# Optimization experiments

Measured on AMD Instinct MI355X. Metric: run time of the kernel, lower is better.

The kernel has to match this reference:

```python
import jax, jax.numpy as jnp
import numpy as np

D_K = 64

def setup_inputs() -> dict:
    key = jax.random.key(0)
    kq, kk, kv = jax.random.split(key, 3)
    shape = (2, 16, 2048, D_K)  # [B, H, S, d_k]
    q = jax.random.normal(kq, shape, dtype=jnp.float32)
    k = jax.random.normal(kk, shape, dtype=jnp.float32)
    v = jax.random.normal(kv, shape, dtype=jnp.float32)
    return {"q": q, "k": k, "v": v}

def reference(q, k, v):
    # score = q @ k^T / sqrt(d_k)  -> [B, H, S, S]
    scale = 1.0 / np.sqrt(D_K).astype(np.float32)
    score = jnp.einsum("bhqd,bhkd->bhqk", q, k) * scale
    attn = jax.nn.softmax(score, axis=-1)
    # dropout is identity in eval mode
    out = jnp.einsum("bhqk,bhkd->bhqd", attn, v)
    return out
```

## Files before the change

kernel.cpp:

```cpp
#include <hip/hip_runtime.h>
#include <hip/hip_bf16.h>
#include <math.h>
#include <stdint.h>


#define S_LEN 2048
#define DK 64
#define QW 32
#define NW 4
#define QBLK (QW * NW)
#define KVBLK 64
#define NT (S_LEN / KVBLK)
#define LOG2E 1.44269504088896340736f
#define THR 8.0f

typedef __attribute__((ext_vector_type(16))) float f32x16;
typedef __attribute__((ext_vector_type(8)))  __bf16 bf16x8;
typedef __attribute__((ext_vector_type(4)))  __bf16 bf16x4;
typedef __attribute__((ext_vector_type(4)))  uint32_t u32x4;

union frag_cast { u32x4 u; bf16x8 h; };

__device__ __forceinline__ uint32_t cvt_pk_bf16(float lo, float hi) {
    uint32_t r;
    asm("v_cvt_pk_bf16_f32 %0, %1, %2" : "=v"(r) : "v"(lo), "v"(hi));
    return r;
}
__device__ __forceinline__ void perm32swap(uint32_t& a, uint32_t& b) {
    asm volatile("v_permlane32_swap_b32 %0, %1" : "+v"(a), "+v"(b));
}
__device__ __forceinline__ void load_lds16(const __bf16* g, __bf16* l) {
    __builtin_amdgcn_global_load_lds(
        (const __attribute__((address_space(1))) void*)g,
        (__attribute__((address_space(3))) void*)l, 16, 0, 0);
}
__device__ __forceinline__ bf16x8 pack8(float4 a, float4 b) {
    bf16x8 f;
    f[0] = (__bf16)a.x; f[1] = (__bf16)a.y; f[2] = (__bf16)a.z; f[3] = (__bf16)a.w;
    f[4] = (__bf16)b.x; f[5] = (__bf16)b.y; f[6] = (__bf16)b.z; f[7] = (__bf16)b.w;
    return f;
}

__global__ __launch_bounds__(256)
void prep_pack(const float* __restrict__ Kg, const float* __restrict__ Vg,
               __bf16* __restrict__ Kimg, __bf16* __restrict__ Vimg)
{
    __shared__ float Vs[64 * 65];
    const int tid = threadIdx.x;
    const int t = blockIdx.x, bh = blockIdx.y;
    const size_t ibase = ((size_t)bh * S_LEN + (size_t)t * 64) * DK;
    const size_t obase = ((size_t)bh * NT + t) * 4096;

    #pragma unroll
    for (int u = 0; u < 2; ++u) {
        const int rho = tid + 256 * u;
        const int r = rho >> 3, j = rho & 7;
        const float* src = Kg + ibase + r * 64 + j * 8;
        float4 a = *(const float4*)(src);
        float4 b = *(const float4*)(src + 4);
        *(bf16x8*)(Kimg + obase + r * 64 + ((j * 8) ^ ((r & 7) << 3))) = pack8(a, b);
    }

    {
        const int r = tid >> 2, c0 = (tid & 3) * 16;
        const float* src = Vg + ibase + r * 64 + c0;
        #pragma unroll
        for (int m = 0; m < 4; ++m) {
            float4 x = *(const float4*)(src + 4 * m);
            float* dst = &Vs[r * 65 + c0 + 4 * m];
            dst[0] = x.x; dst[1] = x.y; dst[2] = x.z; dst[3] = x.w;
        }
    }
    __syncthreads();
    #pragma unroll
    for (int u = 0; u < 2; ++u) {
        const int rho = tid + 256 * u;
        const int d = rho >> 3, j = rho & 7;
        const int k0 = 8 * (j ^ (d & 7));
        bf16x8 wv;
        #pragma unroll
        for (int i = 0; i < 8; ++i) wv[i] = (__bf16)Vs[(k0 + i) * 65 + d];
        *(bf16x8*)(Vimg + obase + d * 64 + j * 8) = wv;
    }
}

__global__ __launch_bounds__(256, 2)
void attn_fwd_lds(const float* __restrict__ Qg, const __bf16* __restrict__ Kimg,
                  const __bf16* __restrict__ Vimg, float* __restrict__ Og)
{
    __shared__ __align__(16) __bf16 Kl[2][4096];
    __shared__ __align__(16) __bf16 Vt[2][4096];

    const int tid = threadIdx.x;
    const int lane = tid & 63;
    const int w   = tid >> 6;
    const int l31 = lane & 31;
    const int hi  = lane >> 5;

    const int qt = blockIdx.x;
    const int bh = blockIdx.y;
    const size_t base = (size_t)bh * (S_LEN * DK);
    const int q0g = qt * QBLK + w * QW;

    bf16x8 qf[4];
    {
        const float sc = 0.125f * LOG2E;
        const float* qrow = Qg + base + (size_t)(q0g + l31) * DK;
        #pragma unroll
        for (int sp = 0; sp < 4; ++sp) {
            const int d0 = 16 * sp + 8 * hi;
            float4 a = *(const float4*)(qrow + d0);
            float4 b = *(const float4*)(qrow + d0 + 4);
            bf16x8 f;
            f[0] = (__bf16)(a.x * sc); f[1] = (__bf16)(a.y * sc);
            f[2] = (__bf16)(a.z * sc); f[3] = (__bf16)(a.w * sc);
            f[4] = (__bf16)(b.x * sc); f[5] = (__bf16)(b.y * sc);
            f[6] = (__bf16)(b.z * sc); f[7] = (__bf16)(b.w * sc);
            qf[sp] = f;
        }
    }

    f32x16 acc0 = {}, acc1 = {};
    float m_run = -INFINITY, l_run = 0.f;

    const __bf16* kbase = Kimg + (size_t)bh * NT * 4096;
    const __bf16* vbase = Vimg + (size_t)bh * NT * 4096;

    auto stage = [&](int t, int b) {
        const __bf16* kt = kbase + (size_t)t * 4096 + tid * 8;
        const __bf16* vt = vbase + (size_t)t * 4096 + tid * 8;
        load_lds16(kt,        &Kl[b][w * 512]);
        load_lds16(kt + 2048, &Kl[b][2048 + w * 512]);
        load_lds16(vt,        &Vt[b][w * 512]);
        load_lds16(vt + 2048, &Vt[b][2048 + w * 512]);
    };

    stage(0, 0);
    __syncthreads();

    int cur = 0;
    #pragma unroll 1
    for (int t = 0; t < NT; ++t) {
        if (t + 1 < NT) stage(t + 1, cur ^ 1);

        f32x16 s0 = {}, s1 = {};
        __builtin_amdgcn_s_setprio(1);
        #pragma unroll
        for (int sp = 0; sp < 4; ++sp) {
            #pragma unroll
            for (int kt2 = 0; kt2 < 2; ++kt2) {
                const int krow = kt2 * 32 + l31;
                const int eo = krow * 64 + ((16 * sp + 8 * hi) ^ ((krow & 7) << 3));
                bf16x8 kb = *(const bf16x8*)(&Kl[cur][eo]);
                if (kt2 == 0) s0 = __builtin_amdgcn_mfma_f32_32x32x16_bf16(kb, qf[sp], s0, 0, 0, 0);
                else          s1 = __builtin_amdgcn_mfma_f32_32x32x16_bf16(kb, qf[sp], s1, 0, 0, 0);
            }
        }
        __builtin_amdgcn_s_setprio(0);

        float vmax = -INFINITY;
        #pragma unroll
        for (int j = 0; j < 16; ++j) vmax = fmaxf(vmax, s0[j]);
        #pragma unroll
        for (int j = 0; j < 16; ++j) vmax = fmaxf(vmax, s1[j]);
        vmax = fmaxf(vmax, __shfl_xor(vmax, 32));

        if (!__all(vmax - m_run <= THR)) {
            const float mnew = fmaxf(m_run, vmax);
            const float alpha = __builtin_amdgcn_exp2f(m_run - mnew);
            m_run = mnew;
            l_run *= alpha;
            #pragma unroll
            for (int r = 0; r < 16; ++r) {
                const int ql = (r & 3) + 8 * (r >> 2) + 4 * hi;
                const float ar = __shfl(alpha, ql + (hi << 5));
                acc0[r] *= ar;
                acc1[r] *= ar;
            }
        }

        float rs = 0.f;
        #pragma unroll
        for (int j = 0; j < 16; ++j) { const float p = __builtin_amdgcn_exp2f(s0[j] - m_run); s0[j] = p; rs += p; }
        #pragma unroll
        for (int j = 0; j < 16; ++j) { const float p = __builtin_amdgcn_exp2f(s1[j] - m_run); s1[j] = p; rs += p; }
        rs += __shfl_xor(rs, 32);
        l_run += rs;

        frag_cast pa[4];
        #pragma unroll
        for (int b2 = 0; b2 < 2; ++b2) {
            #pragma unroll
            for (int st = 0; st < 2; ++st) {
                uint32_t wa, wb, wc, wd;
                if (b2 == 0) {
                    wa = cvt_pk_bf16(s0[8 * st + 0], s0[8 * st + 1]);
                    wb = cvt_pk_bf16(s0[8 * st + 2], s0[8 * st + 3]);
                    wc = cvt_pk_bf16(s0[8 * st + 4], s0[8 * st + 5]);
                    wd = cvt_pk_bf16(s0[8 * st + 6], s0[8 * st + 7]);
                } else {
                    wa = cvt_pk_bf16(s1[8 * st + 0], s1[8 * st + 1]);
                    wb = cvt_pk_bf16(s1[8 * st + 2], s1[8 * st + 3]);
                    wc = cvt_pk_bf16(s1[8 * st + 4], s1[8 * st + 5]);
                    wd = cvt_pk_bf16(s1[8 * st + 6], s1[8 * st + 7]);
                }
                perm32swap(wa, wc);
                perm32swap(wb, wd);
                pa[2 * b2 + st].u = (u32x4){wa, wb, wc, wd};
            }
        }

        __builtin_amdgcn_s_setprio(1);
        #pragma unroll
        for (int ks = 0; ks < 4; ++ks) {
            #pragma unroll
            for (int dt = 0; dt < 2; ++dt) {
                const int d = dt * 32 + l31;
                const int eo = d * 64 + ((16 * ks + 8 * hi) ^ ((d & 7) << 3));
                bf16x8 vb = *(const bf16x8*)(&Vt[cur][eo]);
                if (dt == 0) acc0 = __builtin_amdgcn_mfma_f32_32x32x16_bf16(pa[ks].h, vb, acc0, 0, 0, 0);
                else         acc1 = __builtin_amdgcn_mfma_f32_32x32x16_bf16(pa[ks].h, vb, acc1, 0, 0, 0);
            }
        }
        __builtin_amdgcn_s_setprio(0);

        __syncthreads();
        cur ^= 1;
    }

    float* op = Og + base;
    #pragma unroll
    for (int r = 0; r < 16; ++r) {
        const int ql = (r & 3) + 8 * (r >> 2) + 4 * hi;
        const float lr = __shfl(l_run, ql + (hi << 5));
        const float invl = 1.0f / lr;
        const size_t row = (size_t)(q0g + ql) * DK;
        op[row + l31]      = acc0[r] * invl;
        op[row + 32 + l31] = acc1[r] * invl;
    }
}

__global__ __launch_bounds__(256, 2)
void attn_fwd_fb(const float* __restrict__ Qg, const float* __restrict__ Kg,
                 const float* __restrict__ Vg, float* __restrict__ Og)
{
    __shared__ __align__(16) __bf16 Kl[2][64 * 64];
    __shared__ __align__(16) __bf16 Vt[2][64 * 64];

    const int tid = threadIdx.x;
    const int lane = tid & 63;
    const int w   = tid >> 6;
    const int l31 = lane & 31;
    const int hi  = lane >> 5;

    const int qt = blockIdx.x;
    const int bh = blockIdx.y;
    const size_t base = (size_t)bh * (S_LEN * DK);
    const int q0g = qt * QBLK + w * QW;

    bf16x8 qf[4];
    {
        const float sc = 0.125f * LOG2E;
        const float* qrow = Qg + base + (size_t)(q0g + l31) * DK;
        #pragma unroll
        for (int sp = 0; sp < 4; ++sp) {
            const int d0 = 16 * sp + 8 * hi;
            float4 a = *(const float4*)(qrow + d0);
            float4 b = *(const float4*)(qrow + d0 + 4);
            bf16x8 f;
            f[0] = (__bf16)(a.x * sc); f[1] = (__bf16)(a.y * sc);
            f[2] = (__bf16)(a.z * sc); f[3] = (__bf16)(a.w * sc);
            f[4] = (__bf16)(b.x * sc); f[5] = (__bf16)(b.y * sc);
            f[6] = (__bf16)(b.z * sc); f[7] = (__bf16)(b.w * sc);
            qf[sp] = f;
        }
    }

    f32x16 acc0 = {}, acc1 = {};
    float m_run = -INFINITY, l_run = 0.f;

    float4 kpre[4];
    float  vpre[4][4];
    const int vd  = tid & 63;
    const int vkq = tid >> 6;

    auto issueLoads = [&](int t) {
        const int kv0 = t * KVBLK;
        #pragma unroll
        for (int i = 0; i < 4; ++i) {
            const int idx = tid + 256 * i;
            const int r = idx >> 4, c = idx & 15;
            kpre[i] = *(const float4*)(Kg + base + (size_t)(kv0 + r) * DK + c * 4);
        }
        #pragma unroll
        for (int i = 0; i < 4; ++i) {
            const int k0 = vkq * 4 + 16 * i;
            const float* vp = Vg + base + (size_t)(kv0 + k0) * DK + vd;
            vpre[i][0] = vp[0];      vpre[i][1] = vp[DK];
            vpre[i][2] = vp[2 * DK]; vpre[i][3] = vp[3 * DK];
        }
    };
    auto writeTile = [&](int b) {
        #pragma unroll
        for (int i = 0; i < 4; ++i) {
            const int idx = tid + 256 * i;
            const int r = idx >> 4, c = idx & 15;
            bf16x4 pk;
            pk[0] = (__bf16)kpre[i].x; pk[1] = (__bf16)kpre[i].y;
            pk[2] = (__bf16)kpre[i].z; pk[3] = (__bf16)kpre[i].w;
            *(bf16x4*)(&Kl[b][r * 64 + ((c * 4) ^ ((r & 7) << 3))]) = pk;
        }
        #pragma unroll
        for (int i = 0; i < 4; ++i) {
            const int k0 = vkq * 4 + 16 * i;
            bf16x4 pv;
            pv[0] = (__bf16)vpre[i][0]; pv[1] = (__bf16)vpre[i][1];
            pv[2] = (__bf16)vpre[i][2]; pv[3] = (__bf16)vpre[i][3];
            *(bf16x4*)(&Vt[b][vd * 64 + (k0 ^ ((vd & 7) << 3))]) = pv;
        }
    };

    issueLoads(0);
    writeTile(0);
    __syncthreads();

    int cur = 0;
    #pragma unroll 1
    for (int t = 0; t < NT; ++t) {
        if (t + 1 < NT) issueLoads(t + 1);

        f32x16 s0 = {}, s1 = {};
        __builtin_amdgcn_s_setprio(1);
        #pragma unroll
        for (int sp = 0; sp < 4; ++sp) {
            #pragma unroll
            for (int kt2 = 0; kt2 < 2; ++kt2) {
                const int krow = kt2 * 32 + l31;
                const int eo = krow * 64 + ((16 * sp + 8 * hi) ^ ((krow & 7) << 3));
                bf16x8 kb = *(const bf16x8*)(&Kl[cur][eo]);
                if (kt2 == 0) s0 = __builtin_amdgcn_mfma_f32_32x32x16_bf16(kb, qf[sp], s0, 0, 0, 0);
                else          s1 = __builtin_amdgcn_mfma_f32_32x32x16_bf16(kb, qf[sp], s1, 0, 0, 0);
            }
        }
        __builtin_amdgcn_s_setprio(0);

        float vmax = -INFINITY;
        #pragma unroll
        for (int j = 0; j < 16; ++j) vmax = fmaxf(vmax, s0[j]);
        #pragma unroll
        for (int j = 0; j < 16; ++j) vmax = fmaxf(vmax, s1[j]);
        vmax = fmaxf(vmax, __shfl_xor(vmax, 32));

        if (!__all(vmax - m_run <= THR)) {
            const float mnew = fmaxf(m_run, vmax);
            const float alpha = __builtin_amdgcn_exp2f(m_run - mnew);
            m_run = mnew;
            l_run *= alpha;
            #pragma unroll
            for (int r = 0; r < 16; ++r) {
                const int ql = (r & 3) + 8 * (r >> 2) + 4 * hi;
                const float ar = __shfl(alpha, ql + (hi << 5));
                acc0[r] *= ar;
                acc1[r] *= ar;
            }
        }

        float rs = 0.f;
        #pragma unroll
        for (int j = 0; j < 16; ++j) { const float p = __builtin_amdgcn_exp2f(s0[j] - m_run); s0[j] = p; rs += p; }
        #pragma unroll
        for (int j = 0; j < 16; ++j) { const float p = __builtin_amdgcn_exp2f(s1[j] - m_run); s1[j] = p; rs += p; }
        rs += __shfl_xor(rs, 32);
        l_run += rs;

        frag_cast pa[4];
        #pragma unroll
        for (int b2 = 0; b2 < 2; ++b2) {
            #pragma unroll
            for (int st = 0; st < 2; ++st) {
                uint32_t wa, wb, wc, wd;
                if (b2 == 0) {
                    wa = cvt_pk_bf16(s0[8 * st + 0], s0[8 * st + 1]);
                    wb = cvt_pk_bf16(s0[8 * st + 2], s0[8 * st + 3]);
                    wc = cvt_pk_bf16(s0[8 * st + 4], s0[8 * st + 5]);
                    wd = cvt_pk_bf16(s0[8 * st + 6], s0[8 * st + 7]);
                } else {
                    wa = cvt_pk_bf16(s1[8 * st + 0], s1[8 * st + 1]);
                    wb = cvt_pk_bf16(s1[8 * st + 2], s1[8 * st + 3]);
                    wc = cvt_pk_bf16(s1[8 * st + 4], s1[8 * st + 5]);
                    wd = cvt_pk_bf16(s1[8 * st + 6], s1[8 * st + 7]);
                }
                perm32swap(wa, wc);
                perm32swap(wb, wd);
                pa[2 * b2 + st].u = (u32x4){wa, wb, wc, wd};
            }
        }

        __builtin_amdgcn_s_setprio(1);
        #pragma unroll
        for (int ks = 0; ks < 4; ++ks) {
            #pragma unroll
            for (int dt = 0; dt < 2; ++dt) {
                const int d = dt * 32 + l31;
                const int eo = d * 64 + ((16 * ks + 8 * hi) ^ ((d & 7) << 3));
                bf16x8 vb = *(const bf16x8*)(&Vt[cur][eo]);
                if (dt == 0) acc0 = __builtin_amdgcn_mfma_f32_32x32x16_bf16(pa[ks].h, vb, acc0, 0, 0, 0);
                else         acc1 = __builtin_amdgcn_mfma_f32_32x32x16_bf16(pa[ks].h, vb, acc1, 0, 0, 0);
            }
        }
        __builtin_amdgcn_s_setprio(0);

        if (t + 1 < NT) writeTile(cur ^ 1);
        __syncthreads();
        cur ^= 1;
    }

    float* op = Og + base;
    #pragma unroll
    for (int r = 0; r < 16; ++r) {
        const int ql = (r & 3) + 8 * (r >> 2) + 4 * hi;
        const float lr = __shfl(l_run, ql + (hi << 5));
        const float invl = 1.0f / lr;
        const size_t row = (size_t)(q0g + ql) * DK;
        op[row + l31]      = acc0[r] * invl;
        op[row + 32 + l31] = acc1[r] * invl;
    }
}

extern "C" void kernel_launch(void* const* d_in, const int* in_sizes, int n_in,
                              void* d_out, int out_size, void* d_ws, size_t ws_size,
                              hipStream_t stream) {
    const float* q = (const float*)d_in[0];
    const float* k = (const float*)d_in[1];
    const float* v = (const float*)d_in[2];
    float* o = (float*)d_out;
    const int bh = in_sizes[0] / (S_LEN * DK);

    const size_t img_bytes = (size_t)bh * NT * 4096 * sizeof(__bf16);
    if (ws_size >= 2 * img_bytes) {
        __bf16* Kimg = (__bf16*)d_ws;
        __bf16* Vimg = (__bf16*)((char*)d_ws + img_bytes);
        prep_pack<<<dim3(NT, bh), dim3(256), 0, stream>>>(k, v, Kimg, Vimg);
        attn_fwd_lds<<<dim3(S_LEN / QBLK, bh), dim3(256), 0, stream>>>(q, Kimg, Vimg, o);
    } else {
        attn_fwd_fb<<<dim3(S_LEN / QBLK, bh), dim3(256), 0, stream>>>(q, k, v, o);
    }
}
```

Measured before the change: 67.53 us.

## Pre-pack K/V in MFMA fragment order and compute row sums via MFMA

```diff
diff --git a/kernel.cpp b/kernel.cpp
--- a/kernel.cpp
+++ b/kernel.cpp
@@ -52,13 +52,16 @@
     const size_t obase = ((size_t)bh * NT + t) * 4096;
 
     #pragma unroll
-    for (int u = 0; u < 2; ++u) {
-        const int rho = tid + 256 * u;
-        const int r = rho >> 3, j = rho & 7;
-        const float* src = Kg + ibase + r * 64 + j * 8;
+    for (int u0 = 0; u0 < 2; ++u0) {
+        const int u = tid + 256 * u0;
+        const int f = u >> 6, lane = u & 63;
+        const int sp = f >> 1, kt2 = f & 1;
+        const int row = kt2 * 32 + (lane & 31);
+        const int col = 16 * sp + 8 * (lane >> 5);
+        const float* src = Kg + ibase + row * 64 + col;
         float4 a = *(const float4*)(src);
         float4 b = *(const float4*)(src + 4);
-        *(bf16x8*)(Kimg + obase + r * 64 + ((j * 8) ^ ((r & 7) << 3))) = pack8(a, b);
+        *(bf16x8*)(Kimg + obase + (size_t)u * 8) = pack8(a, b);
     }
 
     {
@@ -73,14 +76,16 @@
     }
     __syncthreads();
     #pragma unroll
-    for (int u = 0; u < 2; ++u) {
-        const int rho = tid + 256 * u;
-        const int d = rho >> 3, j = rho & 7;
-        const int k0 = 8 * (j ^ (d & 7));
+    for (int u0 = 0; u0 < 2; ++u0) {
+        const int u = tid + 256 * u0;
+        const int g = u >> 6, lane = u & 63;
+        const int ks = g >> 1, dt = g & 1;
+        const int k0 = 16 * ks + 8 * (lane >> 5);
+        const int d  = dt * 32 + (lane & 31);
         bf16x8 wv;
         #pragma unroll
         for (int i = 0; i < 8; ++i) wv[i] = (__bf16)Vs[(k0 + i) * 65 + d];
-        *(bf16x8*)(Vimg + obase + d * 64 + j * 8) = wv;
+        *(bf16x8*)(Vimg + obase + (size_t)u * 8) = wv;
     }
 }
 
@@ -120,11 +125,16 @@
         }
     }
 
-    f32x16 acc0 = {}, acc1 = {};
-    float m_run = -INFINITY, l_run = 0.f;
+    bf16x8 ones;
+    #pragma unroll
+    for (int i = 0; i < 8; ++i) ones[i] = (__bf16)1.0f;
+
+    f32x16 acc0 = {}, acc1 = {}, acc2 = {};
+    float m_run = -INFINITY;
 
     const __bf16* kbase = Kimg + (size_t)bh * NT * 4096;
     const __bf16* vbase = Vimg + (size_t)bh * NT * 4096;
+    const int loff = lane * 8;
 
     auto stage = [&](int t, int b) {
         const __bf16* kt = kbase + (size_t)t * 4096 + tid * 8;
@@ -147,45 +157,41 @@
         __builtin_amdgcn_s_setprio(1);
         #pragma unroll
         for (int sp = 0; sp < 4; ++sp) {
-            #pragma unroll
-            for (int kt2 = 0; kt2 < 2; ++kt2) {
-                const int krow = kt2 * 32 + l31;
-                const int eo = krow * 64 + ((16 * sp + 8 * hi) ^ ((krow & 7) << 3));
-                bf16x8 kb = *(const bf16x8*)(&Kl[cur][eo]);
-                if (kt2 == 0) s0 = __builtin_amdgcn_mfma_f32_32x32x16_bf16(kb, qf[sp], s0, 0, 0, 0);
-                else          s1 = __builtin_amdgcn_mfma_f32_32x32x16_bf16(kb, qf[sp], s1, 0, 0, 0);
-            }
+            bf16x8 kb0 = *(const bf16x8*)(&Kl[cur][(sp * 2 + 0) * 512 + loff]);
+            bf16x8 kb1 = *(const bf16x8*)(&Kl[cur][(sp * 2 + 1) * 512 + loff]);
+            s0 = __builtin_amdgcn_mfma_f32_32x32x16_bf16(kb0, qf[sp], s0, 0, 0, 0);
+            s1 = __builtin_amdgcn_mfma_f32_32x32x16_bf16(kb1, qf[sp], s1, 0, 0, 0);
         }
         __builtin_amdgcn_s_setprio(0);
 
-        float vmax = -INFINITY;
-        #pragma unroll
-        for (int j = 0; j < 16; ++j) vmax = fmaxf(vmax, s0[j]);
-        #pragma unroll
-        for (int j = 0; j < 16; ++j) vmax = fmaxf(vmax, s1[j]);
+        float a16[16];
+        #pragma unroll
+        for (int j = 0; j < 16; ++j) a16[j] = fmaxf(s0[j], s1[j]);
+        float vmax = fmaxf(fmaxf(a16[0], a16[1]), a16[2]);
+        #pragma unroll
+        for (int j = 0; j < 6; ++j)
+            vmax = fmaxf(fmaxf(vmax, a16[3 + 2 * j]), a16[4 + 2 * j]);
+        vmax = fmaxf(vmax, a16[15]);
         vmax = fmaxf(vmax, __shfl_xor(vmax, 32));
 
         if (!__all(vmax - m_run <= THR)) {
             const float mnew = fmaxf(m_run, vmax);
             const float alpha = __builtin_amdgcn_exp2f(m_run - mnew);
             m_run = mnew;
-            l_run *= alpha;
             #pragma unroll
             for (int r = 0; r < 16; ++r) {
                 const int ql = (r & 3) + 8 * (r >> 2) + 4 * hi;
                 const float ar = __shfl(alpha, ql + (hi << 5));
                 acc0[r] *= ar;
                 acc1[r] *= ar;
-            }
-        }
-
-        float rs = 0.f;
-        #pragma unroll
-        for (int j = 0; j < 16; ++j) { const float p = __builtin_amdgcn_exp2f(s0[j] - m_run); s0[j] = p; rs += p; }
-        #pragma unroll
-        for (int j = 0; j < 16; ++j) { const float p = __builtin_amdgcn_exp2f(s1[j] - m_run); s1[j] = p; rs += p; }
-        rs += __shfl_xor(rs, 32);
-        l_run += rs;
+                acc2[r] *= ar;
+            }
+        }
+
+        #pragma unroll
+        for (int j = 0; j < 16; ++j) s0[j] = __builtin_amdgcn_exp2f(s0[j] - m_run);
+        #pragma unroll
+        for (int j = 0; j < 16; ++j) s1[j] = __builtin_amdgcn_exp2f(s1[j] - m_run);
 
         frag_cast pa[4];
         #pragma unroll
@@ -213,14 +219,11 @@
         __builtin_amdgcn_s_setprio(1);
         #pragma unroll
         for (int ks = 0; ks < 4; ++ks) {
-            #pragma unroll
-            for (int dt = 0; dt < 2; ++dt) {
-                const int d = dt * 32 + l31;
-                const int eo = d * 64 + ((16 * ks + 8 * hi) ^ ((d & 7) << 3));
-                bf16x8 vb = *(const bf16x8*)(&Vt[cur][eo]);
-                if (dt == 0) acc0 = __builtin_amdgcn_mfma_f32_32x32x16_bf16(pa[ks].h, vb, acc0, 0, 0, 0);
-                else         acc1 = __builtin_amdgcn_mfma_f32_32x32x16_bf16(pa[ks].h, vb, acc1, 0, 0, 0);
-            }
+            bf16x8 vb0 = *(const bf16x8*)(&Vt[cur][(ks * 2 + 0) * 512 + loff]);
+            bf16x8 vb1 = *(const bf16x8*)(&Vt[cur][(ks * 2 + 1) * 512 + loff]);
+            acc0 = __builtin_amdgcn_mfma_f32_32x32x16_bf16(pa[ks].h, vb0, acc0, 0, 0, 0);
+            acc1 = __builtin_amdgcn_mfma_f32_32x32x16_bf16(pa[ks].h, vb1, acc1, 0, 0, 0);
+            acc2 = __builtin_amdgcn_mfma_f32_32x32x16_bf16(pa[ks].h, ones, acc2, 0, 0, 0);
         }
         __builtin_amdgcn_s_setprio(0);
 
@@ -232,8 +235,7 @@
     #pragma unroll
     for (int r = 0; r < 16; ++r) {
         const int ql = (r & 3) + 8 * (r >> 2) + 4 * hi;
-        const float lr = __shfl(l_run, ql + (hi << 5));
-        const float invl = 1.0f / lr;
+        const float invl = 1.0f / acc2[r];
         const size_t row = (size_t)(q0g + ql) * DK;
         op[row + l31]      = acc0[r] * invl;
         op[row + 32 + l31] = acc1[r] * invl;
```

Result: no change. 68.24 us (+1.1%).
